# Kernel optimization log

Hardware: AMD Instinct MI355X
Metric: run time of the kernel (lower is better)

## Reference

```python
import jax, jax.numpy as jnp
import numpy as np

D_MODEL = 1024
NUM_HEADS = 16
HEAD_DIM = D_MODEL // NUM_HEADS  # 64
N = 1024
B = 8


def setup_inputs() -> dict:
    key = jax.random.key(0)
    ks = jax.random.split(key, 11)
    s = 0.02
    inp = {
        'query': jax.random.normal(ks[0], (B, D_MODEL, N), jnp.float32),
        'key':   jax.random.normal(ks[1], (B, D_MODEL, N), jnp.float32),
        'value': jax.random.normal(ks[2], (B, D_MODEL, N), jnp.float32),
        # 1x1 conv1d == linear over channel dim: weight [out, in], bias [out]
        'Wq': jax.random.normal(ks[3], (D_MODEL, D_MODEL), jnp.float32) * s,
        'bq': jax.random.normal(ks[4], (D_MODEL,), jnp.float32) * s,
        'Wk': jax.random.normal(ks[5], (D_MODEL, D_MODEL), jnp.float32) * s,
        'bk': jax.random.normal(ks[6], (D_MODEL,), jnp.float32) * s,
        'Wv': jax.random.normal(ks[7], (D_MODEL, D_MODEL), jnp.float32) * s,
        'bv': jax.random.normal(ks[8], (D_MODEL,), jnp.float32) * s,
        'Wm': jax.random.normal(ks[9], (D_MODEL, D_MODEL), jnp.float32) * s,
        'bm': jax.random.normal(ks[10], (D_MODEL,), jnp.float32) * s,
    }
    return inp


def _proj(W, b, x):
    # nn.Conv1d(kernel_size=1): out[b,o,n] = sum_i W[o,i] x[b,i,n] + b[o]
    return jnp.einsum('oi,bin->bon', W, x) + b[None, :, None]


def reference(query, key, value, Wq, bq, Wk, bk, Wv, bv, Wm, bm):
    Bd = query.shape[0]
    # view(B, dim, heads, N): channel axis split as (head_dim, num_heads)
    q = _proj(Wq, bq, query).reshape(Bd, HEAD_DIM, NUM_HEADS, -1)
    k = _proj(Wk, bk, key).reshape(Bd, HEAD_DIM, NUM_HEADS, -1)
    v = _proj(Wv, bv, value).reshape(Bd, HEAD_DIM, NUM_HEADS, -1)
    scale = 1.0 / (HEAD_DIM ** 0.5)
    scores = jnp.einsum('bdhn,bdhm->bhnm', q, k) * scale  # [B,H,N,N]
    prob = jax.nn.softmax(scores, axis=-1)
    x = jnp.einsum('bhnm,bdhm->bdhn', prob, v)  # [B,D,H,N]
    out = _proj(Wm, bm, x.reshape(Bd, HEAD_DIM * NUM_HEADS, -1))
    return out
```

## Files before the change

### kernel.cpp

```cpp
#include <hip/hip_runtime.h>

typedef __bf16 bf16x8 __attribute__((ext_vector_type(8)));
typedef __bf16 bf16x4 __attribute__((ext_vector_type(4)));
typedef float f32x4 __attribute__((ext_vector_type(4)));
typedef unsigned short u16;
typedef unsigned int u32;

typedef union { bf16x8 v8; bf16x4 v4[2]; } bfu;

__device__ __forceinline__ u16 f2bf(float f) {
  u32 u = __builtin_bit_cast(u32, f);
  u = (u + 0x7FFFu + ((u >> 16) & 1u)) >> 16;
  return (u16)u;
}

__device__ __forceinline__ void gload_lds16(const void* g, void* l) {
  __builtin_amdgcn_global_load_lds((const __attribute__((address_space(1))) void*)g,
                                   (__attribute__((address_space(3))) void*)l, 16, 0, 0);
}

__global__ __launch_bounds__(256) void transpose_cast3(const float* __restrict__ q,
                                                       const float* __restrict__ k,
                                                       const float* __restrict__ v,
                                                       u16* __restrict__ X3) {
  __shared__ float T[64][68];
  int tid = threadIdx.x;
  int n0 = blockIdx.x * 64, i0 = blockIdx.y * 64;
  int z = blockIdx.z;
  int which = z >> 3, b = z & 7;
  const float* src = (which == 0) ? q : (which == 1) ? k : v;
  size_t boff = (size_t)b << 20;
  const float* s = src + boff;
  u16* d = X3 + ((size_t)which << 23) + boff;
  int ir = tid >> 4, n4 = (tid & 15) * 4;
#pragma unroll
  for (int r = 0; r < 4; ++r) {
    int i_loc = ir + r * 16;
    float4 vv = *(const float4*)(s + (size_t)(i0 + i_loc) * 1024 + n0 + n4);
    *(float4*)&T[i_loc][n4] = vv;
  }
  __syncthreads();
  int nr = tid >> 3, i8 = (tid & 7) * 8;
#pragma unroll
  for (int r = 0; r < 2; ++r) {
    int n_loc = nr + r * 32;
    u32 pk[4];
#pragma unroll
    for (int j = 0; j < 4; ++j) {
      float f0 = T[i8 + 2 * j][n_loc];
      float f1 = T[i8 + 2 * j + 1][n_loc];
      pk[j] = (u32)f2bf(f0) | ((u32)f2bf(f1) << 16);
    }
    *(uint4*)(d + (size_t)(n0 + n_loc) * 1024 + i0 + i8) = make_uint4(pk[0], pk[1], pk[2], pk[3]);
  }
}

__global__ __launch_bounds__(256) void transpose_cast(const float* __restrict__ src,
                                                      u16* __restrict__ dst) {
  __shared__ float T[64][68];
  int tid = threadIdx.x;
  int n0 = blockIdx.x * 64, i0 = blockIdx.y * 64;
  size_t boff = (size_t)blockIdx.z << 20;
  const float* s = src + boff;
  u16* d = dst + boff;
  int ir = tid >> 4, n4 = (tid & 15) * 4;
#pragma unroll
  for (int r = 0; r < 4; ++r) {
    int i_loc = ir + r * 16;
    float4 v = *(const float4*)(s + (size_t)(i0 + i_loc) * 1024 + n0 + n4);
    *(float4*)&T[i_loc][n4] = v;
  }
  __syncthreads();
  int nr = tid >> 3, i8 = (tid & 7) * 8;
#pragma unroll
  for (int r = 0; r < 2; ++r) {
    int n_loc = nr + r * 32;
    u32 pk[4];
#pragma unroll
    for (int j = 0; j < 4; ++j) {
      float f0 = T[i8 + 2 * j][n_loc];
      float f1 = T[i8 + 2 * j + 1][n_loc];
      pk[j] = (u32)f2bf(f0) | ((u32)f2bf(f1) << 16);
    }
    *(uint4*)(d + (size_t)(n0 + n_loc) * 1024 + i0 + i8) = make_uint4(pk[0], pk[1], pk[2], pk[3]);
  }
}

__global__ __launch_bounds__(256) void cast_weights(const float* __restrict__ Wq,
                                                    const float* __restrict__ Wk,
                                                    const float* __restrict__ Wv,
                                                    const float* __restrict__ Wm,
                                                    u16* __restrict__ out) {
  int w = blockIdx.y;
  const float* src = (w == 0) ? Wq : (w == 1) ? Wk : (w == 2) ? Wv : Wm;
  u16* dst = out + ((size_t)w << 20);
  int o = blockIdx.x;
  int c4 = threadIdx.x * 4;
  float f[4];
  if (w < 3) {
    float4 v = *(const float4*)(src + (size_t)o * 1024 + c4);
    f[0] = v.x; f[1] = v.y; f[2] = v.z; f[3] = v.w;
  } else {
#pragma unroll
    for (int j = 0; j < 4; ++j) {
      int cp = c4 + j;
      f[j] = src[(size_t)o * 1024 + (cp & 63) * 16 + (cp >> 6)];
    }
  }
  u32 p0 = (u32)f2bf(f[0]) | ((u32)f2bf(f[1]) << 16);
  u32 p1 = (u32)f2bf(f[2]) | ((u32)f2bf(f[3]) << 16);
  *(uint2*)(dst + (size_t)o * 1024 + c4) = make_uint2(p0, p1);
}

__device__ __forceinline__ void gemm_body(const u16* __restrict__ A,
                                          const u16* __restrict__ B,
                                          const float* __restrict__ bias,
                                          void* __restrict__ Out, float escale,
                                          int epi, u16* LD) {
  int tid = threadIdx.x;
  int wave = tid >> 6, l = tid & 63, ln = l & 15, g = l >> 4;
  int wm = wave >> 1, wn = wave & 1;
  int bid = blockIdx.x;
  int mt = (bid >> 3) & 7;
  int nt = ((bid & 7) << 2) | (bid >> 6);
  int c0 = mt * 128, n0 = nt * 256;

  int R = tid >> 3;
  int v = (tid & 7) ^ (R & 7);
  const u16* aS = A + (size_t)(c0 + 2 * R + (v >> 2)) * 1024 + (v & 3) * 8;
  const u16* bS = B + (size_t)(n0 + 2 * R + (v >> 2)) * 1024 + (v & 3) * 8;

  int slr = ((((ln & 1) << 2) | g) ^ ((ln >> 1) & 7)) * 8;
  int laneA = (wm * 32 + (ln >> 1)) * 64 + slr;
  int laneB = (wn * 64 + (ln >> 1)) * 64 + slr;

  f32x4 acc[4][8] = {};

#define STAGE(buf, kt)                                                        \
  do {                                                                        \
    gload_lds16(aS + (kt) * 32, &LD[(buf) * 4096 + tid * 8]);                 \
    gload_lds16(aS + 65536 + (kt) * 32, &LD[(buf) * 4096 + 2048 + tid * 8]);  \
    gload_lds16(bS + (kt) * 32, &LD[12288 + (buf) * 8192 + tid * 8]);         \
    gload_lds16(bS + 65536 + (kt) * 32,                                       \
                &LD[12288 + (buf) * 8192 + 2048 + tid * 8]);                  \
    gload_lds16(bS + 131072 + (kt) * 32,                                      \
                &LD[12288 + (buf) * 8192 + 4096 + tid * 8]);                  \
    gload_lds16(bS + 196608 + (kt) * 32,                                      \
                &LD[12288 + (buf) * 8192 + 6144 + tid * 8]);                  \
  } while (0)

  STAGE(0, 0);
  STAGE(1, 1);

#pragma unroll
  for (int t = 0; t < 32; ++t) {
    if (t < 31)
      asm volatile("s_waitcnt vmcnt(6)" ::: "memory");
    else
      asm volatile("s_waitcnt vmcnt(0)" ::: "memory");
    asm volatile("s_barrier" ::: "memory");
    if (t <= 29) STAGE((t + 2) % 3, t + 2);
    const int ab = (t % 3) * 4096;
    const int bb = 12288 + (t % 3) * 8192;
    bf16x8 af[4];
#pragma unroll
    for (int mm = 0; mm < 4; ++mm) af[mm] = *(const bf16x8*)&LD[ab + laneA + mm * 512];
    __builtin_amdgcn_s_setprio(1);
#pragma unroll
    for (int nn = 0; nn < 8; ++nn) {
      bf16x8 bfr = *(const bf16x8*)&LD[bb + laneB + nn * 512];
#pragma unroll
      for (int mm = 0; mm < 4; ++mm)
        acc[mm][nn] = __builtin_amdgcn_mfma_f32_16x16x32_bf16(af[mm], bfr, acc[mm][nn], 0, 0, 0);
    }
    __builtin_amdgcn_s_setprio(0);
  }
#undef STAGE

  int D0 = (c0 >> 4) + wm * 4;
#pragma unroll
  for (int nn = 0; nn < 8; ++nn) {
    size_t ng = (size_t)n0 + wn * 128 + nn * 16 + ln;
#pragma unroll
    for (int r = 0; r < 4; ++r) {
      int h = g * 4 + r;
      if (epi == 0) {
        bf16x4 pk;
#pragma unroll
        for (int mm = 0; mm < 4; ++mm) {
          int c = c0 + wm * 64 + mm * 16 + h;
          pk[mm] = (__bf16)((acc[mm][nn][r] + bias[c]) * escale);
        }
        *(bf16x4*)((u16*)Out + ng * 1024 + (size_t)h * 64 + D0) = pk;
      } else {
        size_t b = ng >> 10, n = ng & 1023;
#pragma unroll
        for (int mm = 0; mm < 4; ++mm) {
          int c = c0 + wm * 64 + mm * 16 + h;
          float val = (acc[mm][nn][r] + bias[c]) * escale;
          if (epi == 1) {
            int d = D0 + mm;
            ((u16*)Out)[((b * 16 + h) * 64 + d) * 1024 + n] = f2bf(val);
          } else {
            ((float*)Out)[(b << 20) + (size_t)c * 1024 + n] = val;
          }
        }
      }
    }
  }
}

template <int EPI>
__global__ __launch_bounds__(256, 2) void gemm4b(const u16* __restrict__ A,
                                                 const u16* __restrict__ B,
                                                 const float* __restrict__ bias,
                                                 void* __restrict__ Out, float escale) {
  __shared__ u16 LD[36864];
  gemm_body(A, B, bias, Out, escale, EPI, LD);
}

__device__ __forceinline__ void gemm8_body(const u16* __restrict__ A,
                                           const u16* __restrict__ B,
                                           const float* __restrict__ bias,
                                           void* __restrict__ Out, float escale,
                                           int epi, u16* LD) {
  int tid = threadIdx.x;
  int wave = tid >> 6, l = tid & 63, ln = l & 15, g = l >> 4;
  int wm = wave >> 2, wn = wave & 3;
  int bid = blockIdx.x;
  int j = bid >> 3;
  int mt = j & 3;
  int nt = (bid & 7) * 8 + (j >> 2);
  int c0 = mt * 256, n0 = nt * 128;

  int r0 = tid >> 2;
  int sw = ((tid & 3) ^ ((tid >> 3) & 3)) * 8;
  const u16* aS = A + (size_t)(c0 + r0) * 1024 + sw;
  const u16* bS = B + (size_t)(n0 + r0 % 128) * 1024 + sw;
  int dst0 = tid * 8;

  int swr = (g ^ ((ln >> 1) & 3)) * 8;
  int laneA = (wm * 128 + ln) * 32 + swr;
  int laneB = 32768 + (wn * 32 + ln) * 32 + swr;

  f32x4 acc[8][2] = {};

#define SUA(kkv, kt, buf)                                                 \
  do {                                                                    \
    const u16* s_ = aS + (kt) * 64 + (kkv) * 32;                          \
    int d_ = (buf) * 16384 + (kkv) * 8192 + dst0;                         \
    gload_lds16(s_, &LD[d_]);                                             \
    gload_lds16(s_ + 131072, &LD[d_ + 4096]);                             \
  } while (0)
#define SUB(kkv, kt, buf)                                                 \
  do {                                                                    \
    gload_lds16(bS + (kt) * 64 + (kkv) * 32,                              \
                &LD[32768 + (buf) * 8192 + (kkv) * 4096 + dst0]);         \
  } while (0)

  SUA(0, 0, 0);
  SUB(0, 0, 0);
  SUA(1, 0, 0);
  SUB(1, 0, 0);

#pragma unroll
  for (int kt = 0; kt < 16; ++kt) {
    const int buf = kt & 1;
    const int ab = buf * 16384;
    const int bb = buf * 8192;
    bf16x8 af[4], bf0[2];
    asm volatile("s_waitcnt vmcnt(3)" ::: "memory");
    asm volatile("s_barrier" ::: "memory");
#pragma unroll
    for (int m = 0; m < 4; ++m) af[m] = *(const bf16x8*)&LD[ab + laneA + m * 512];
#pragma unroll
    for (int nn = 0; nn < 2; ++nn) bf0[nn] = *(const bf16x8*)&LD[bb + laneB + nn * 512];
    if (kt < 15) SUA(0, kt + 1, buf ^ 1);
    __builtin_amdgcn_s_setprio(1);
#pragma unroll
    for (int m = 0; m < 4; ++m)
#pragma unroll
      for (int nn = 0; nn < 2; ++nn)
        acc[m][nn] = __builtin_amdgcn_mfma_f32_16x16x32_bf16(af[m], bf0[nn], acc[m][nn], 0, 0, 0);
    __builtin_amdgcn_s_setprio(0);
#pragma unroll
    for (int m = 0; m < 4; ++m) af[m] = *(const bf16x8*)&LD[ab + laneA + (m + 4) * 512];
    if (kt < 15) SUB(0, kt + 1, buf ^ 1);
    __builtin_amdgcn_s_setprio(1);
#pragma unroll
    for (int m = 0; m < 4; ++m)
#pragma unroll
      for (int nn = 0; nn < 2; ++nn)
        acc[m + 4][nn] = __builtin_amdgcn_mfma_f32_16x16x32_bf16(af[m], bf0[nn], acc[m + 4][nn], 0, 0, 0);
    __builtin_amdgcn_s_setprio(0);
    if (kt < 15)
      asm volatile("s_waitcnt vmcnt(3)" ::: "memory");
    else
      asm volatile("s_waitcnt vmcnt(0)" ::: "memory");
    asm volatile("s_barrier" ::: "memory");
#pragma unroll
    for (int m = 0; m < 4; ++m) af[m] = *(const bf16x8*)&LD[ab + 8192 + laneA + m * 512];
#pragma unroll
    for (int nn = 0; nn < 2; ++nn) bf0[nn] = *(const bf16x8*)&LD[bb + 4096 + laneB + nn * 512];
    if (kt < 15) SUA(1, kt + 1, buf ^ 1);
    __builtin_amdgcn_s_setprio(1);
#pragma unroll
    for (int m = 0; m < 4; ++m)
#pragma unroll
      for (int nn = 0; nn < 2; ++nn)
        acc[m][nn] = __builtin_amdgcn_mfma_f32_16x16x32_bf16(af[m], bf0[nn], acc[m][nn], 0, 0, 0);
    __builtin_amdgcn_s_setprio(0);
#pragma unroll
    for (int m = 0; m < 4; ++m) af[m] = *(const bf16x8*)&LD[ab + 8192 + laneA + (m + 4) * 512];
    if (kt < 15) SUB(1, kt + 1, buf ^ 1);
    __builtin_amdgcn_s_setprio(1);
#pragma unroll
    for (int m = 0; m < 4; ++m)
#pragma unroll
      for (int nn = 0; nn < 2; ++nn)
        acc[m + 4][nn] = __builtin_amdgcn_mfma_f32_16x16x32_bf16(af[m], bf0[nn], acc[m + 4][nn], 0, 0, 0);
    __builtin_amdgcn_s_setprio(0);
  }
#undef SUA
#undef SUB

  int D0 = (c0 >> 4) + wm * 8;
#pragma unroll
  for (int nn = 0; nn < 2; ++nn) {
    size_t ng = (size_t)n0 + wn * 32 + nn * 16 + ln;
#pragma unroll
    for (int r = 0; r < 4; ++r) {
      int h = g * 4 + r;
      if (epi == 0) {
        bf16x8 pk;
#pragma unroll
        for (int m = 0; m < 8; ++m) {
          int c = c0 + wm * 128 + m * 16 + h;
          pk[m] = (__bf16)((acc[m][nn][r] + bias[c]) * escale);
        }
        *(bf16x8*)((u16*)Out + ng * 1024 + (size_t)h * 64 + D0) = pk;
      } else {
        size_t b = ng >> 10, n = ng & 1023;
#pragma unroll
        for (int m = 0; m < 8; ++m) {
          int c = c0 + wm * 128 + m * 16 + h;
          float val = (acc[m][nn][r] + bias[c]) * escale;
          if (epi == 1) {
            int d = D0 + m;
            ((u16*)Out)[((b * 16 + h) * 64 + d) * 1024 + n] = f2bf(val);
          } else {
            ((float*)Out)[(b << 20) + (size_t)c * 1024 + n] = val;
          }
        }
      }
    }
  }
}

__global__ __launch_bounds__(512, 1) void gemm_qkv8(const u16* __restrict__ Wbf,
                                                    const u16* __restrict__ X3,
                                                    const float* __restrict__ bq,
                                                    const float* __restrict__ bk,
                                                    const float* __restrict__ bv,
                                                    u16* __restrict__ Qh,
                                                    u16* __restrict__ Kh,
                                                    u16* __restrict__ Vt, float qscale) {
  __shared__ u16 LD[49152];
  int z = blockIdx.y;
  const u16* A = Wbf + ((size_t)z << 20);
  const u16* B = X3 + ((size_t)z << 23);
  const float* bias = (z == 0) ? bq : (z == 1) ? bk : bv;
  void* Out = (z == 0) ? (void*)Qh : (z == 1) ? (void*)Kh : (void*)Vt;
  float escale = (z == 0) ? qscale : 1.0f;
  int epi = (z == 2) ? 1 : 0;
  gemm8_body(A, B, bias, Out, escale, epi, LD);
}

__global__ __launch_bounds__(512, 1) void gemm8f(const u16* __restrict__ A,
                                                 const u16* __restrict__ B,
                                                 const float* __restrict__ bias,
                                                 void* __restrict__ Out) {
  __shared__ u16 LD[49152];
  gemm8_body(A, B, bias, Out, 1.0f, 2, LD);
}

__global__ __launch_bounds__(256, 2) void attn_kernel(const u16* __restrict__ Qh,
                                                      const u16* __restrict__ Kh,
                                                      const u16* __restrict__ Vt,
                                                      u16* __restrict__ Xh) {
  __shared__ u16 Ks[2][4096];
  __shared__ u16 Vs[2][4096];
  int tid = threadIdx.x;
  int w = tid >> 6, l = tid & 63, ln = l & 15, g = l >> 4;
  int id = blockIdx.x;
  int bh7 = id & 7;
  int qp = (id >> 3) & 3;
  int bh = (id >> 5) * 8 + bh7;
  size_t b = bh >> 4;
  int h = bh & 15;
  const u16* Qg = Qh + (b << 20) + (h << 6);
  const u16* Kg = Kh + (b << 20) + (h << 6);
  const u16* Vg = Vt + ((size_t)bh << 16);
  u16* Og = Xh + (b << 20) + (h << 6);

  bf16x8 qf[4][2];
#pragma unroll
  for (int t = 0; t < 4; ++t)
#pragma unroll
    for (int kk = 0; kk < 2; ++kk)
      qf[t][kk] = *(const bf16x8*)(Qg + (size_t)(qp * 256 + t * 64 + w * 16 + ln) * 1024 + kk * 32 + g * 8);

  int lr = l >> 3;
  int sw8 = ((l & 7) ^ lr) << 3;
  int r0 = w * 16 + lr, r1 = r0 + 8;
  const u16* kS0 = Kg + (size_t)r0 * 1024 + sw8;
  const u16* kS1 = Kg + (size_t)r1 * 1024 + sw8;
  const u16* vS0 = Vg + (size_t)r0 * 1024 + sw8;
  const u16* vS1 = Vg + (size_t)r1 * 1024 + sw8;

  f32x4 xacc[4][4] = {};
  float lacc[4] = {0.f, 0.f, 0.f, 0.f};

  gload_lds16(kS0, &Ks[0][(w * 2) * 512]);
  gload_lds16(kS1, &Ks[0][(w * 2 + 1) * 512]);
  gload_lds16(vS0, &Vs[0][(w * 2) * 512]);
  gload_lds16(vS1, &Vs[0][(w * 2 + 1) * 512]);
  __syncthreads();

  int sx = ln & 7;
  int cur = 0;
  for (int kt = 0; kt < 16; ++kt) {
    if (kt < 15) {
      int nxt = cur ^ 1;
      gload_lds16(kS0 + (size_t)(kt + 1) * 65536, &Ks[nxt][(w * 2) * 512]);
      gload_lds16(kS1 + (size_t)(kt + 1) * 65536, &Ks[nxt][(w * 2 + 1) * 512]);
      gload_lds16(vS0 + (kt + 1) * 64, &Vs[nxt][(w * 2) * 512]);
      gload_lds16(vS1 + (kt + 1) * 64, &Vs[nxt][(w * 2 + 1) * 512]);
    }
    bf16x8 kf[2][4];
#pragma unroll
    for (int kk = 0; kk < 2; ++kk)
#pragma unroll
      for (int f = 0; f < 4; ++f) {
        int slot = (((kk << 2) + g) ^ sx) << 3;
        kf[kk][f] = *(const bf16x8*)&Ks[cur][(f * 16 + ln) * 64 + slot];
      }
    bf16x8 vf[2][4];
#pragma unroll
    for (int kk = 0; kk < 2; ++kk) {
      int s0 = (kk << 2) + (g >> 1);
      int off = (g & 1) << 2;
#pragma unroll
      for (int fd = 0; fd < 4; ++fd) {
        int rowb = (fd * 16 + ln) * 64;
        bfu uv;
        uv.v4[0] = *(const bf16x4*)&Vs[cur][rowb + ((s0 ^ sx) << 3) + off];
        uv.v4[1] = *(const bf16x4*)&Vs[cur][rowb + (((s0 + 2) ^ sx) << 3) + off];
        vf[kk][fd] = uv.v8;
      }
    }
#pragma unroll
    for (int t = 0; t < 4; ++t) {
      f32x4 sacc[4] = {};
#pragma unroll
      for (int kk = 0; kk < 2; ++kk)
#pragma unroll
        for (int f = 0; f < 4; ++f)
          sacc[f] = __builtin_amdgcn_mfma_f32_16x16x32_bf16(kf[kk][f], qf[t][kk], sacc[f], 0, 0, 0);
      bf16x8 pf[2];
#pragma unroll
      for (int kk = 0; kk < 2; ++kk) {
        bfu up;
#pragma unroll
        for (int e2 = 0; e2 < 2; ++e2) {
          int f = 2 * kk + e2;
          float p0 = __builtin_amdgcn_exp2f(sacc[f][0]);
          float p1 = __builtin_amdgcn_exp2f(sacc[f][1]);
          float p2 = __builtin_amdgcn_exp2f(sacc[f][2]);
          float p3 = __builtin_amdgcn_exp2f(sacc[f][3]);
          lacc[t] += (p0 + p1) + (p2 + p3);
          bf16x4 pb;
          pb[0] = (__bf16)p0; pb[1] = (__bf16)p1; pb[2] = (__bf16)p2; pb[3] = (__bf16)p3;
          up.v4[e2] = pb;
        }
        pf[kk] = up.v8;
      }
#pragma unroll
      for (int kk = 0; kk < 2; ++kk)
#pragma unroll
        for (int fd = 0; fd < 4; ++fd)
          xacc[t][fd] = __builtin_amdgcn_mfma_f32_16x16x32_bf16(pf[kk], vf[kk][fd], xacc[t][fd], 0, 0, 0);
    }
    __syncthreads();
    cur ^= 1;
  }

#pragma unroll
  for (int t = 0; t < 4; ++t) {
    float lt = lacc[t];
    lt += __shfl_xor(lt, 16);
    lt += __shfl_xor(lt, 32);
    float il[4];
#pragma unroll
    for (int r = 0; r < 4; ++r) il[r] = 1.0f / __shfl(lt, g * 4 + r);
#pragma unroll
    for (int fd = 0; fd < 4; ++fd)
#pragma unroll
      for (int r = 0; r < 4; ++r) {
        int nq = qp * 256 + t * 64 + w * 16 + g * 4 + r;
        Og[(size_t)nq * 1024 + fd * 16 + ln] = f2bf(xacc[t][fd][r] * il[r]);
      }
  }
}

extern "C" void kernel_launch(void* const* d_in, const int* in_sizes, int n_in,
                              void* d_out, int out_size, void* d_ws, size_t ws_size,
                              hipStream_t stream) {
  const float* q  = (const float*)d_in[0];
  const float* k  = (const float*)d_in[1];
  const float* v  = (const float*)d_in[2];
  const float* Wq = (const float*)d_in[3];
  const float* bq = (const float*)d_in[4];
  const float* Wk = (const float*)d_in[5];
  const float* bk = (const float*)d_in[6];
  const float* Wv = (const float*)d_in[7];
  const float* bv = (const float*)d_in[8];
  const float* Wm = (const float*)d_in[9];
  const float* bm = (const float*)d_in[10];

  char* ws = (char*)d_ws;
  u16* Wbf = (u16*)ws;
  u16* Qh  = (u16*)(ws + (8ull << 20));
  u16* Kh  = (u16*)(ws + (24ull << 20));
  u16* Vt  = (u16*)(ws + (40ull << 20));
  u16* X3  = (u16*)(ws + (56ull << 20));

  cast_weights<<<dim3(1024, 4, 1), 256, 0, stream>>>(Wq, Wk, Wv, Wm, Wbf);

  const float qscale = 0.125f * 1.44269504088896340736f;

  if (ws_size >= (104ull << 20)) {
    transpose_cast3<<<dim3(16, 16, 24), 256, 0, stream>>>(q, k, v, X3);
    gemm_qkv8<<<dim3(256, 3), 512, 0, stream>>>(Wbf, X3, bq, bk, bv, Qh, Kh, Vt, qscale);
    attn_kernel<<<512, 256, 0, stream>>>(Qh, Kh, Vt, X3);
    gemm8f<<<256, 512, 0, stream>>>(Wbf + (3u << 20), X3, bm, d_out);
  } else {
    dim3 tg(16, 16, 8);
    transpose_cast<<<tg, 256, 0, stream>>>(q, X3);
    gemm4b<0><<<256, 256, 0, stream>>>(Wbf, X3, bq, Qh, qscale);
    transpose_cast<<<tg, 256, 0, stream>>>(k, X3);
    gemm4b<0><<<256, 256, 0, stream>>>(Wbf + (1u << 20), X3, bk, Kh, 1.0f);
    transpose_cast<<<tg, 256, 0, stream>>>(v, X3);
    gemm4b<1><<<256, 256, 0, stream>>>(Wbf + (2u << 20), X3, bv, Vt, 1.0f);
    attn_kernel<<<512, 256, 0, stream>>>(Qh, Kh, Vt, X3);
    gemm4b<2><<<256, 256, 0, stream>>>(Wbf + (3u << 20), X3, bm, d_out, 1.0f);
  }
}
```

Baseline: 164.6 us.

## Split K across wave pairs in 8-wave GEMM with triple-buffered LDS staging

Reworks the 8-wave projection GEMM so that pairs of waves split the K=64 slice of each tile. Each wave computes a 128x64 sub-tile over half of K and the partial sums are reduced through LDS at the end. Staging moves from double to triple buffering with a two-tile prefetch distance, and a wider swizzle is used for 64-element rows. This gives each wave larger per-fragment reuse (8x4 accumulators) and deeper memory latency hiding, at the cost of more LDS (144KB), more accumulator registers, and an extra reduction step through LDS.

```diff
diff --git a/kernel.cpp b/kernel.cpp
--- a/kernel.cpp
+++ b/kernel.cpp
@@ -219,115 +219,117 @@
   gemm_body(A, B, bias, Out, escale, EPI, LD);
 }
 
-__device__ __forceinline__ void gemm8_body(const u16* __restrict__ A,
-                                           const u16* __restrict__ B,
-                                           const float* __restrict__ bias,
-                                           void* __restrict__ Out, float escale,
-                                           int epi, u16* LD) {
+__device__ __forceinline__ void gemm_kk_body(const u16* __restrict__ A,
+                                             const u16* __restrict__ B,
+                                             const float* __restrict__ bias,
+                                             void* __restrict__ Out, float escale,
+                                             int epi, u16* LD) {
   int tid = threadIdx.x;
   int wave = tid >> 6, l = tid & 63, ln = l & 15, g = l >> 4;
-  int wm = wave >> 2, wn = wave & 3;
+  int kkw = wave & 1, wn = (wave >> 1) & 1, wm = wave >> 2;
   int bid = blockIdx.x;
   int j = bid >> 3;
   int mt = j & 3;
   int nt = (bid & 7) * 8 + (j >> 2);
   int c0 = mt * 256, n0 = nt * 128;
 
-  int r0 = tid >> 2;
-  int sw = ((tid & 3) ^ ((tid >> 3) & 3)) * 8;
-  const u16* aS = A + (size_t)(c0 + r0) * 1024 + sw;
-  const u16* bS = B + (size_t)(n0 + r0 % 128) * 1024 + sw;
+  int r0 = tid >> 3, sl = tid & 7;
+  int scol = (sl ^ (r0 & 7)) * 8;
+  const u16* aS = A + (size_t)(c0 + r0) * 1024 + scol;
+  const u16* bS = B + (size_t)(n0 + r0) * 1024 + scol;
   int dst0 = tid * 8;
 
-  int swr = (g ^ ((ln >> 1) & 3)) * 8;
-  int laneA = (wm * 128 + ln) * 32 + swr;
-  int laneB = 32768 + (wn * 32 + ln) * 32 + swr;
-
-  f32x4 acc[8][2] = {};
-
-#define SUA(kkv, kt, buf)                                                 \
+  int swr = (((kkw << 2) | g) ^ (ln & 7)) * 8;
+  int laneA = (wm * 128 + ln) * 64 + swr;
+  int laneB = (wn * 64 + ln) * 64 + swr;
+
+  f32x4 acc[8][4] = {};
+
+#define STGA(kt, buf)                                                     \
   do {                                                                    \
-    const u16* s_ = aS + (kt) * 64 + (kkv) * 32;                          \
-    int d_ = (buf) * 16384 + (kkv) * 8192 + dst0;                         \
+    const u16* s_ = aS + (kt) * 64;                                       \
+    int d_ = (buf) * 16384 + dst0;                                        \
     gload_lds16(s_, &LD[d_]);                                             \
-    gload_lds16(s_ + 131072, &LD[d_ + 4096]);                             \
+    gload_lds16(s_ + 65536, &LD[d_ + 4096]);                              \
+    gload_lds16(s_ + 131072, &LD[d_ + 8192]);                             \
+    gload_lds16(s_ + 196608, &LD[d_ + 12288]);                            \
   } while (0)
-#define SUB(kkv, kt, buf)                                                 \
+#define STGB(kt, buf)                                                     \
   do {                                                                    \
-    gload_lds16(bS + (kt) * 64 + (kkv) * 32,                              \
-                &LD[32768 + (buf) * 8192 + (kkv) * 4096 + dst0]);         \
+    const u16* s_ = bS + (kt) * 64;                                       \
+    int d_ = 49152 + (buf) * 8192 + dst0;                                 \
+    gload_lds16(s_, &LD[d_]);                                             \
+    gload_lds16(s_ + 65536, &LD[d_ + 4096]);                              \
   } while (0)
 
-  SUA(0, 0, 0);
-  SUB(0, 0, 0);
-  SUA(1, 0, 0);
-  SUB(1, 0, 0);
-
-#pragma unroll
-  for (int kt = 0; kt < 16; ++kt) {
-    const int buf = kt & 1;
-    const int ab = buf * 16384;
-    const int bb = buf * 8192;
-    bf16x8 af[4], bf0[2];
-    asm volatile("s_waitcnt vmcnt(3)" ::: "memory");
-    asm volatile("s_barrier" ::: "memory");
-#pragma unroll
-    for (int m = 0; m < 4; ++m) af[m] = *(const bf16x8*)&LD[ab + laneA + m * 512];
-#pragma unroll
-    for (int nn = 0; nn < 2; ++nn) bf0[nn] = *(const bf16x8*)&LD[bb + laneB + nn * 512];
-    if (kt < 15) SUA(0, kt + 1, buf ^ 1);
-    __builtin_amdgcn_s_setprio(1);
-#pragma unroll
-    for (int m = 0; m < 4; ++m)
-#pragma unroll
-      for (int nn = 0; nn < 2; ++nn)
-        acc[m][nn] = __builtin_amdgcn_mfma_f32_16x16x32_bf16(af[m], bf0[nn], acc[m][nn], 0, 0, 0);
-    __builtin_amdgcn_s_setprio(0);
-#pragma unroll
-    for (int m = 0; m < 4; ++m) af[m] = *(const bf16x8*)&LD[ab + laneA + (m + 4) * 512];
-    if (kt < 15) SUB(0, kt + 1, buf ^ 1);
-    __builtin_amdgcn_s_setprio(1);
-#pragma unroll
-    for (int m = 0; m < 4; ++m)
-#pragma unroll
-      for (int nn = 0; nn < 2; ++nn)
-        acc[m + 4][nn] = __builtin_amdgcn_mfma_f32_16x16x32_bf16(af[m], bf0[nn], acc[m + 4][nn], 0, 0, 0);
-    __builtin_amdgcn_s_setprio(0);
-    if (kt < 15)
-      asm volatile("s_waitcnt vmcnt(3)" ::: "memory");
+  STGA(0, 0);
+  STGB(0, 0);
+  STGA(1, 1);
+  STGB(1, 1);
+
+#pragma unroll
+  for (int t = 0; t < 16; ++t) {
+    if (t < 15)
+      asm volatile("s_waitcnt vmcnt(6)" ::: "memory");
     else
       asm volatile("s_waitcnt vmcnt(0)" ::: "memory");
     asm volatile("s_barrier" ::: "memory");
-#pragma unroll
-    for (int m = 0; m < 4; ++m) af[m] = *(const bf16x8*)&LD[ab + 8192 + laneA + m * 512];
-#pragma unroll
-    for (int nn = 0; nn < 2; ++nn) bf0[nn] = *(const bf16x8*)&LD[bb + 4096 + laneB + nn * 512];
-    if (kt < 15) SUA(1, kt + 1, buf ^ 1);
+    const int ab = (t % 3) * 16384;
+    const int bb = 49152 + (t % 3) * 8192;
+    bf16x8 af[4], bfr[4];
+#pragma unroll
+    for (int m = 0; m < 4; ++m) af[m] = *(const bf16x8*)&LD[ab + laneA + m * 1024];
+#pragma unroll
+    for (int nn = 0; nn < 4; ++nn) bfr[nn] = *(const bf16x8*)&LD[bb + laneB + nn * 1024];
+    if (t <= 13) STGA(t + 2, (t + 2) % 3);
     __builtin_amdgcn_s_setprio(1);
 #pragma unroll
     for (int m = 0; m < 4; ++m)
 #pragma unroll
-      for (int nn = 0; nn < 2; ++nn)
-        acc[m][nn] = __builtin_amdgcn_mfma_f32_16x16x32_bf16(af[m], bf0[nn], acc[m][nn], 0, 0, 0);
+      for (int nn = 0; nn < 4; ++nn)
+        acc[m][nn] = __builtin_amdgcn_mfma_f32_16x16x32_bf16(af[m], bfr[nn], acc[m][nn], 0, 0, 0);
     __builtin_amdgcn_s_setprio(0);
 #pragma unroll
-    for (int m = 0; m < 4; ++m) af[m] = *(const bf16x8*)&LD[ab + 8192 + laneA + (m + 4) * 512];
-    if (kt < 15) SUB(1, kt + 1, buf ^ 1);
+    for (int m = 0; m < 4; ++m) af[m] = *(const bf16x8*)&LD[ab + laneA + (m + 4) * 1024];
+    if (t <= 13) STGB(t + 2, (t + 2) % 3);
     __builtin_amdgcn_s_setprio(1);
 #pragma unroll
     for (int m = 0; m < 4; ++m)
 #pragma unroll
-      for (int nn = 0; nn < 2; ++nn)
-        acc[m + 4][nn] = __builtin_amdgcn_mfma_f32_16x16x32_bf16(af[m], bf0[nn], acc[m + 4][nn], 0, 0, 0);
+      for (int nn = 0; nn < 4; ++nn)
+        acc[m + 4][nn] = __builtin_amdgcn_mfma_f32_16x16x32_bf16(af[m], bfr[nn], acc[m + 4][nn], 0, 0, 0);
     __builtin_amdgcn_s_setprio(0);
   }
-#undef SUA
-#undef SUB
+#undef STGA
+#undef STGB
+
+  float* LDf = (float*)LD;
+  int mybase = wave * 4160 + l * 65;
+  int pbase = (wave ^ 1) * 4160 + l * 65;
+  __syncthreads();
+#pragma unroll
+  for (int m = 0; m < 8; ++m)
+#pragma unroll
+    for (int p = 0; p < 2; ++p) {
+      int nn = 2 * (1 - kkw) + p;
+      *(f32x4*)&LDf[mybase + (m * 2 + p) * 4] = acc[m][nn];
+    }
+  __syncthreads();
+#pragma unroll
+  for (int m = 0; m < 8; ++m)
+#pragma unroll
+    for (int p = 0; p < 2; ++p) {
+      int nn = 2 * kkw + p;
+      f32x4 v = *(const f32x4*)&LDf[pbase + (m * 2 + p) * 4];
+      acc[m][nn][0] += v[0]; acc[m][nn][1] += v[1];
+      acc[m][nn][2] += v[2]; acc[m][nn][3] += v[3];
+    }
 
   int D0 = (c0 >> 4) + wm * 8;
 #pragma unroll
-  for (int nn = 0; nn < 2; ++nn) {
-    size_t ng = (size_t)n0 + wn * 32 + nn * 16 + ln;
+  for (int p = 0; p < 2; ++p) {
+    int nn = 2 * kkw + p;
+    size_t ng = (size_t)n0 + wn * 64 + nn * 16 + ln;
 #pragma unroll
     for (int r = 0; r < 4; ++r) {
       int h = g * 4 + r;
@@ -357,7 +359,7 @@
   }
 }
 
-__global__ __launch_bounds__(512, 1) void gemm_qkv8(const u16* __restrict__ Wbf,
+__global__ __launch_bounds__(512, 1) void gemm_qkvs(const u16* __restrict__ Wbf,
                                                     const u16* __restrict__ X3,
                                                     const float* __restrict__ bq,
                                                     const float* __restrict__ bk,
@@ -365,7 +367,7 @@
                                                     u16* __restrict__ Qh,
                                                     u16* __restrict__ Kh,
                                                     u16* __restrict__ Vt, float qscale) {
-  __shared__ u16 LD[49152];
+  __shared__ u16 LD[73728];
   int z = blockIdx.y;
   const u16* A = Wbf + ((size_t)z << 20);
   const u16* B = X3 + ((size_t)z << 23);
@@ -373,15 +375,15 @@
   void* Out = (z == 0) ? (void*)Qh : (z == 1) ? (void*)Kh : (void*)Vt;
   float escale = (z == 0) ? qscale : 1.0f;
   int epi = (z == 2) ? 1 : 0;
-  gemm8_body(A, B, bias, Out, escale, epi, LD);
-}
-
-__global__ __launch_bounds__(512, 1) void gemm8f(const u16* __restrict__ A,
-                                                 const u16* __restrict__ B,
-                                                 const float* __restrict__ bias,
-                                                 void* __restrict__ Out) {
-  __shared__ u16 LD[49152];
-  gemm8_body(A, B, bias, Out, 1.0f, 2, LD);
+  gemm_kk_body(A, B, bias, Out, escale, epi, LD);
+}
+
+__global__ __launch_bounds__(512, 1) void gemm_fs(const u16* __restrict__ A,
+                                                  const u16* __restrict__ B,
+                                                  const float* __restrict__ bias,
+                                                  void* __restrict__ Out) {
+  __shared__ u16 LD[73728];
+  gemm_kk_body(A, B, bias, Out, 1.0f, 2, LD);
 }
 
 __global__ __launch_bounds__(256, 2) void attn_kernel(const u16* __restrict__ Qh,
@@ -541,9 +543,9 @@
 
   if (ws_size >= (104ull << 20)) {
     transpose_cast3<<<dim3(16, 16, 24), 256, 0, stream>>>(q, k, v, X3);
-    gemm_qkv8<<<dim3(256, 3), 512, 0, stream>>>(Wbf, X3, bq, bk, bv, Qh, Kh, Vt, qscale);
+    gemm_qkvs<<<dim3(256, 3), 512, 0, stream>>>(Wbf, X3, bq, bk, bv, Qh, Kh, Vt, qscale);
     attn_kernel<<<512, 256, 0, stream>>>(Qh, Kh, Vt, X3);
-    gemm8f<<<256, 512, 0, stream>>>(Wbf + (3u << 20), X3, bm, d_out);
+    gemm_fs<<<256, 512, 0, stream>>>(Wbf + (3u << 20), X3, bm, d_out);
   } else {
     dim3 tg(16, 16, 8);
     transpose_cast<<<tg, 256, 0, stream>>>(q, X3);
```

Result: slower. 275.2 us (+67.2%).
